# Kernel optimization log

Hardware: AMD Instinct MI355X
Metric: run time of the kernel (lower is better)

Reference implementation:

```python
import jax, jax.numpy as jnp
import numpy as np


def _quant_dequant_rowwise(v):
    # vector-wise absmax int8 quantization along the last axis, then dequant.
    # Exactly reproduces dequantized result of the int8 GEMM operand:
    # Cx = round(v/s) clipped to [-127,127]; dq = Cx * s.
    s = jnp.max(jnp.abs(v), axis=-1, keepdims=True) / 127.0
    s = jnp.maximum(s, 1e-8)
    q = jnp.clip(jnp.round(v / s), -127.0, 127.0)
    return q * s


def setup_inputs() -> dict:
    key = jax.random.key(0)
    k1, k2, k3 = jax.random.split(key, 3)
    B, S, K, N = 4, 2048, 4096, 4096
    x = jax.random.normal(k1, (B, S, K), dtype=jnp.float32)
    # amplify a few feature columns so |col| exceeds the 6.0 outlier threshold,
    # exercising the LLM.int8() mixed-precision decomposition path
    x = x.at[..., ::256].multiply(10.0)
    W = jax.random.normal(k2, (N, K), dtype=jnp.float32) * 0.02
    bias = jax.random.normal(k3, (N,), dtype=jnp.float32) * 0.01
    return {"x": x, "W": W, "bias": bias, "threshold": 6}


def reference(x, W, bias, threshold):
    # LLM.int8() matmul with outlier decomposition (bnb.matmul semantics):
    #  1. columns of x whose absmax > threshold are outliers -> fp16/fp32 path
    #  2. remaining x columns + full W are vector-wise int8 quantized, int8 GEMM,
    #     dequant with per-row scales (exactly equal to dq(x) @ dq(W).T)
    #  3. out = int8-part + x_outlier @ W_outlier.T + bias
    thr = jnp.asarray(threshold, dtype=x.dtype)
    B_shape = x.shape[:-1]
    K = x.shape[-1]
    x2 = x.reshape(-1, K)                                   # [M, K]
    colmax = jnp.max(jnp.abs(x2), axis=0)                   # [K]
    out_mask = (colmax > thr).astype(x.dtype)               # 1.0 on outlier cols
    x_int = x2 * (1.0 - out_mask)                           # zero outlier cols
    dq_x = _quant_dequant_rowwise(x_int)                    # [M, K]
    dq_w = _quant_dequant_rowwise(W)                        # [N, K]
    out = dq_x @ dq_w.T                                     # int8 GEMM, dequantized
    out = out + (x2 * out_mask) @ (W * out_mask).T          # fp outlier GEMM
    out = out + bias
    return out.reshape(*B_shape, W.shape[0])
```

## Files before the change

kernel.cpp:

```cpp
#include <hip/hip_runtime.h>

typedef unsigned short u16;
typedef unsigned char u8;
typedef unsigned int u32;
typedef __attribute__((ext_vector_type(4))) float f32x4;
typedef __attribute__((ext_vector_type(16))) float f32x16;
typedef __attribute__((ext_vector_type(8))) __bf16 bf16x8;
typedef __attribute__((ext_vector_type(4))) int i32x4;
typedef __attribute__((ext_vector_type(16))) int i32x16;

__device__ __forceinline__ u16 f2bf(float f) {
  u32 u = __float_as_uint(f);
  u32 r = (u + 0x7fffu + ((u >> 16) & 1u)) >> 16;
  return (u16)r;
}

__device__ __forceinline__ float load_thr(const int* p) {
  int iv = *p;
  float fv = __int_as_float(iv);
  if (fv >= 1.0f && fv <= 1.0e6f) return fv;
  return (float)iv;
}

__device__ __forceinline__ void gload_lds16(const void* g, void* l) {
  __builtin_amdgcn_global_load_lds(
      (const __attribute__((address_space(1))) void*)g,
      (__attribute__((address_space(3))) void*)l, 16, 0, 0);
}

__global__ void k_init_cm(u32* cm, int K) {
  int i = blockIdx.x * 256 + threadIdx.x;
  if (i < K) cm[i] = 0u;
}

__global__ __launch_bounds__(256) void k_colmax(const float* __restrict__ x,
                                                u32* __restrict__ cm, int M,
                                                int K, int rpb) {
  int c4 = blockIdx.x * 256 + threadIdx.x;
  int r0 = blockIdx.y * rpb;
  int r1 = r0 + rpb;
  if (r1 > M) r1 = M;
  f32x4 mx = {0.f, 0.f, 0.f, 0.f};
  for (int r = r0; r < r1; ++r) {
    f32x4 v = *(const f32x4*)&x[(size_t)r * K + (size_t)c4 * 4];
#pragma unroll
    for (int i = 0; i < 4; ++i) mx[i] = fmaxf(mx[i], fabsf(v[i]));
  }
#pragma unroll
  for (int i = 0; i < 4; ++i)
    atomicMax(&cm[c4 * 4 + i], __float_as_uint(mx[i]));
}

__global__ void k_ocols(const u32* __restrict__ cm, const int* __restrict__ thr_i,
                        int K, int* __restrict__ meta) {
  int lane = threadIdx.x;
  float thr = load_thr(thr_i);
  const float* cmf = (const float*)cm;
  int per = K >> 6;
  int base = lane * per;
  int c = 0;
  for (int i = 0; i < per; ++i) c += (cmf[base + i] > thr) ? 1 : 0;
  int inc = c;
  for (int off = 1; off < 64; off <<= 1) {
    int t = __shfl_up(inc, off);
    if (lane >= off) inc += t;
  }
  int excl = inc - c;
  int total = __shfl(inc, 63);
  if (lane == 0) meta[0] = total < 64 ? total : 64;
  int idx = excl;
  for (int i = 0; i < per; ++i) {
    if (cmf[base + i] > thr) {
      if (idx < 64) meta[1 + idx] = base + i;
      idx++;
    }
  }
  for (int j = total + lane; j < 64; j += 64) meta[1 + j] = -1;
}

__global__ __launch_bounds__(256) void k_quant8(
    const float* __restrict__ src, const u32* __restrict__ cm,
    const int* __restrict__ thr_i, const int* __restrict__ meta,
    char* __restrict__ qdst, float* __restrict__ sdst, u16* __restrict__ odst,
    int K, int zero_outlier) {
  int row = blockIdx.x;
  int tid = threadIdx.x;
  float thr = load_thr(thr_i);
  const float* sr = src + (size_t)row * K;
  const float* cmf = (const float*)cm;

  float v[16];
  u32 omask = 0;
  float lmax = 0.f;
#pragma unroll
  for (int j = 0; j < 4; ++j) {
    int c4 = j * 256 + tid;
    f32x4 val = *(const f32x4*)&sr[c4 * 4];
    f32x4 cv = *(const f32x4*)&cmf[c4 * 4];
#pragma unroll
    for (int i = 0; i < 4; ++i) {
      float xv = val[i];
      v[j * 4 + i] = xv;
      bool is_out = cv[i] > thr;
      if (is_out) omask |= 1u << (j * 4 + i);
      if (!is_out || !zero_outlier) lmax = fmaxf(lmax, fabsf(xv));
    }
  }
  float m = lmax;
#pragma unroll
  for (int off = 32; off >= 1; off >>= 1) m = fmaxf(m, __shfl_down(m, off));
  __shared__ float red[4];
  int lane = tid & 63, wv = tid >> 6;
  if (lane == 0) red[wv] = m;
  __syncthreads();
  float rm = fmaxf(fmaxf(red[0], red[1]), fmaxf(red[2], red[3]));
  float s = fmaxf(rm / 127.0f, 1e-8f);

  u32* qt = (u32*)qdst;
  size_t rowpart = (size_t)(row >> 5) * (K >> 5) * 256 + (size_t)(row & 31) * 8;
#pragma unroll
  for (int j = 0; j < 4; ++j) {
    int c4 = j * 256 + tid;
    u32 pk = 0;
#pragma unroll
    for (int i = 0; i < 4; ++i) {
      float xv = v[j * 4 + i];
      int iq;
      if (zero_outlier && (omask & (1u << (j * 4 + i)))) {
        iq = 0;
      } else {
        float q = rintf(xv / s);
        q = fminf(fmaxf(q, -127.f), 127.f);
        iq = (int)q;
      }
      pk |= ((u32)(u8)(char)iq) << (8 * i);
    }
    qt[rowpart + (size_t)(c4 >> 3) * 256 + (c4 & 7)] = pk;
  }
  if (tid == 0) sdst[row] = s;
  if (tid < 64) {
    int n_out = meta[0];
    int oc = meta[1 + tid];
    u16 ov = 0;
    if (tid < n_out && oc >= 0) ov = f2bf(sr[oc]);
    odst[(size_t)row * 64 + tid] = ov;
  }
}

__global__ __launch_bounds__(512, 2) void k_gemm_i8(
    const char* __restrict__ qx, const char* __restrict__ qw,
    const float* __restrict__ sx, const float* __restrict__ sw,
    const float* __restrict__ bias, const char* __restrict__ xo,
    const char* __restrict__ wo, float* __restrict__ out, int M, int N,
    int K) {
  extern __shared__ char lds_raw[];
  int tid = threadIdx.x;
  int lane = tid & 63, wave = tid >> 6;
  int wm = wave >> 1, wn = wave & 1;

  int nwg = gridDim.x, bid = blockIdx.x;
  int swzb = (bid & 7) * (nwg >> 3) + (bid >> 3);
  int nbn = N >> 8;
  int bm = swzb / nbn, bn = swzb % nbn;
  int r0 = bm << 8, c0 = bn << 8;
  int K32 = K >> 5;
  int lbyte = (lane & 31) * 32 + (lane >> 5) * 16;

  size_t bpart[4];
  int bg[4];
#pragma unroll
  for (int i = 0; i < 4; ++i) {
    int g = tid + i * 512;
    int b = g >> 6;
    int nb = b >> 2, kb = b & 3;
    bpart[i] = ((size_t)((c0 >> 5) + nb) * K32 + kb) * 1024 + (g & 63) * 16;
    bg[i] = g;
  }
#define STAGE_B(bufp, kt)                                                     \
  {                                                                           \
    _Pragma("unroll") for (int i = 0; i < 4; ++i)                             \
        gload_lds16(qw + bpart[i] + ((size_t)((kt) >> 5) << 10),              \
                    (bufp) + bg[i] * 16);                                     \
  }

  const char* abase0 = qx + ((size_t)((r0 >> 5) + wm * 2) * K32 << 10) + lbyte;
  const char* abase1 = abase0 + ((size_t)K32 << 10);
#define LOAD_A(ar, kt)                                                        \
  {                                                                           \
    _Pragma("unroll") for (int ks = 0; ks < 4; ++ks) {                        \
      ar[ks] = *(const i32x4*)(abase0 + ((size_t)(((kt) >> 5) + ks) << 10));  \
      ar[4 + ks] =                                                            \
          *(const i32x4*)(abase1 + ((size_t)(((kt) >> 5) + ks) << 10));       \
    }                                                                         \
  }

#define BFR(dst, bufp, nf, ks)                                                \
  dst = *(const i32x4*)((bufp) + ((((wn * 4 + (nf)) * 4 + (ks)) << 10)) +     \
                        lbyte);

#define MFI(q, nf, av, bv)                                                    \
  asm volatile("v_mfma_i32_32x32x32_i8 %0, %1, %2, %0"                        \
               : "+v"(acc[q][nf])                                             \
               : "v"(av), "v"(bv))

#define CLUST(ac, p)                                                          \
  {                                                                           \
    __builtin_amdgcn_s_setprio(1);                                            \
    _Pragma("unroll") for (int ks = 0; ks < 4; ++ks) {                        \
      MFI(0, 2 * (p), ac[ks], Bf[ks]);                                        \
      MFI(0, 2 * (p) + 1, ac[ks], Bf[4 + ks]);                                \
      MFI(1, 2 * (p), ac[4 + ks], Bf[ks]);                                    \
      MFI(1, 2 * (p) + 1, ac[4 + ks], Bf[4 + ks]);                            \
    }                                                                         \
    __builtin_amdgcn_s_setprio(0);                                            \
  }

#define TILE(bufc, bufn, ac, an, ktn)                                         \
  {                                                                           \
    STAGE_B(bufn, ktn);                                                       \
    LOAD_A(an, ktn);                                                          \
    __builtin_amdgcn_sched_barrier(0);                                        \
    i32x4 Bf[8];                                                              \
    BFR(Bf[0], bufc, 0, 0); BFR(Bf[1], bufc, 0, 1);                           \
    BFR(Bf[2], bufc, 0, 2); BFR(Bf[3], bufc, 0, 3);                           \
    BFR(Bf[4], bufc, 1, 0); BFR(Bf[5], bufc, 1, 1);                           \
    BFR(Bf[6], bufc, 1, 2); BFR(Bf[7], bufc, 1, 3);                           \
    CLUST(ac, 0);                                                             \
    BFR(Bf[0], bufc, 2, 0); BFR(Bf[1], bufc, 2, 1);                           \
    BFR(Bf[2], bufc, 2, 2); BFR(Bf[3], bufc, 2, 3);                           \
    BFR(Bf[4], bufc, 3, 0); BFR(Bf[5], bufc, 3, 1);                           \
    BFR(Bf[6], bufc, 3, 2); BFR(Bf[7], bufc, 3, 3);                           \
    CLUST(ac, 1);                                                             \
    asm volatile("s_waitcnt vmcnt(0)" ::: "memory");                          \
    __builtin_amdgcn_s_barrier();                                             \
  }

  char* buf0 = lds_raw;
  char* buf1 = lds_raw + 32768;
  i32x16 acc[2][4] = {};
  i32x4 aA[8], aB[8];

  STAGE_B(buf0, 0);
  LOAD_A(aA, 0);
  asm volatile("s_waitcnt vmcnt(0)" ::: "memory");
  __builtin_amdgcn_s_barrier();

  int nit = K / 256;
  for (int it = 0; it < nit; ++it) {
    int kt1 = it * 256 + 128;
    int kt2 = it * 256 + 256;
    kt2 = (kt2 < K) ? kt2 : 0;
    TILE(buf0, buf1, aA, aB, kt1);
    TILE(buf1, buf0, aB, aA, kt2);
  }

#pragma unroll
  for (int i = 0; i < 4; ++i) {
    int g = tid + i * 512;
    int rw = g >> 3;
    int cb = ((g & 7) ^ (rw & 7)) << 4;
    gload_lds16(xo + (size_t)(r0 + rw) * 128 + cb, lds_raw + g * 16);
    gload_lds16(wo + (size_t)(c0 + rw) * 128 + cb, lds_raw + 32768 + g * 16);
  }

  f32x16 facc[2][4];
  float swv[4], bv[4];
#pragma unroll
  for (int nf = 0; nf < 4; ++nf) {
    swv[nf] = sw[c0 + wn * 128 + nf * 32 + (lane & 31)];
    bv[nf] = bias[c0 + wn * 128 + nf * 32 + (lane & 31)];
  }
#pragma unroll
  for (int q = 0; q < 2; ++q) {
    int gmb = r0 + wm * 64 + q * 32 + 4 * (lane >> 5);
    f32x4 s4a = *(const f32x4*)&sx[gmb];
    f32x4 s4b = *(const f32x4*)&sx[gmb + 8];
    f32x4 s4c = *(const f32x4*)&sx[gmb + 16];
    f32x4 s4d = *(const f32x4*)&sx[gmb + 24];
#pragma unroll
    for (int reg = 0; reg < 16; ++reg) {
      float sxv = (reg < 4) ? s4a[reg & 3]
                : (reg < 8) ? s4b[reg & 3]
                : (reg < 12) ? s4c[reg & 3] : s4d[reg & 3];
#pragma unroll
      for (int nf = 0; nf < 4; ++nf)
        facc[q][nf][reg] = (float)acc[q][nf][reg] * sxv * swv[nf];
    }
  }

  asm volatile("s_waitcnt vmcnt(0)" ::: "memory");
  __builtin_amdgcn_s_barrier();

#pragma unroll
  for (int ks = 0; ks < 4; ++ks) {
    bf16x8 ob[4];
#pragma unroll
    for (int nf = 0; nf < 4; ++nf) {
      int rn = wn * 128 + nf * 32 + (lane & 31);
      ob[nf] = *(const bf16x8*)(lds_raw + 32768 + rn * 128 +
                                (((ks * 2 + (lane >> 5)) ^ (rn & 7)) << 4));
    }
#pragma unroll
    for (int q = 0; q < 2; ++q) {
      int rl = wm * 64 + q * 32 + (lane & 31);
      bf16x8 oa = *(const bf16x8*)(lds_raw + rl * 128 +
                                   (((ks * 2 + (lane >> 5)) ^ (rl & 7)) << 4));
#pragma unroll
      for (int nf = 0; nf < 4; ++nf)
        facc[q][nf] = __builtin_amdgcn_mfma_f32_32x32x16_bf16(
            oa, ob[nf], facc[q][nf], 0, 0, 0);
    }
  }

#pragma unroll
  for (int q = 0; q < 2; ++q) {
#pragma unroll
    for (int reg = 0; reg < 16; ++reg) {
      int gm = r0 + wm * 64 + q * 32 + (reg & 3) + 8 * (reg >> 2) +
               4 * (lane >> 5);
      float* orow = out + (size_t)gm * N + c0 + wn * 128 + (lane & 31);
#pragma unroll
      for (int nf = 0; nf < 4; ++nf)
        orow[nf * 32] = facc[q][nf][reg] + bv[nf];
    }
  }
}

extern "C" void kernel_launch(void* const* d_in, const int* in_sizes, int n_in,
                              void* d_out, int out_size, void* d_ws,
                              size_t ws_size, hipStream_t stream) {
  const float* x = (const float*)d_in[0];
  const float* W = (const float*)d_in[1];
  const float* bias = (const float*)d_in[2];
  const int* thr = (const int*)d_in[3];
  float* out = (float*)d_out;

  int N = in_sizes[2];
  int K = in_sizes[1] / N;
  int M = in_sizes[0] / K;

  char* ws = (char*)d_ws;
  u32* cm = (u32*)ws;
  int* meta = (int*)(ws + 16384);
  float* sx = (float*)(ws + 32768);
  float* sw = (float*)(ws + 32768 + (size_t)M * 4);
  char* xo = ws + 32768 + (size_t)(M + N) * 4;
  char* wo = xo + (size_t)M * 128;
  char* qx = wo + (size_t)N * 128;
  char* qw = qx + (size_t)M * K;

  k_init_cm<<<dim3((K + 255) / 256), dim3(256), 0, stream>>>(cm, K);

  {
    int gx = K / 1024;
    int gy = 128;
    int rpb = (M + gy - 1) / gy;
    k_colmax<<<dim3(gx, gy), dim3(256), 0, stream>>>(x, cm, M, K, rpb);
  }

  k_ocols<<<dim3(1), dim3(64), 0, stream>>>(cm, thr, K, meta);

  k_quant8<<<dim3(M), dim3(256), 0, stream>>>(x, cm, thr, meta, qx, sx,
                                              (u16*)xo, K, 1);
  k_quant8<<<dim3(N), dim3(256), 0, stream>>>(W, cm, thr, meta, qw, sw,
                                              (u16*)wo, K, 0);

  (void)hipFuncSetAttribute((const void*)k_gemm_i8,
                            hipFuncAttributeMaxDynamicSharedMemorySize,
                            65536);
  int nwg = (M / 256) * (N / 256);
  k_gemm_i8<<<dim3(nwg), dim3(512), 65536, stream>>>(qx, qw, sx, sw, bias,
                                                     xo, wo, out, M, N, K);
}
```

Baseline: 266.6 us.

## Shrink int8 GEMM tile to 128x256 with 2x4 waves and higher occupancy

Halves the M dimension of each int8 GEMM workgroup tile and rearranges the 8 waves as 2x4, so each wave owns a 64x64 output block with fewer accumulators. The launch bound now targets 4 workgroups per CU. A loads are no longer prefetched a whole tile ahead; they are issued inside each tile in two halves, with explicit waitcnt instructions to overlap them with the MFMAs. An XOR swizzle is added to the quantized operand layout, with matching read offsets, to cut LDS and register-load bank conflicts. The trade-off is twice as many workgroups and less register-level reuse per wave, in exchange for better latency hiding from higher occupancy.

```diff
diff --git a/kernel.cpp b/kernel.cpp
--- a/kernel.cpp
+++ b/kernel.cpp
@@ -118,6 +118,7 @@
 
   u32* qt = (u32*)qdst;
   size_t rowpart = (size_t)(row >> 5) * (K >> 5) * 256 + (size_t)(row & 31) * 8;
+  u32 wxor = ((row >> 2) & 1) << 2;
 #pragma unroll
   for (int j = 0; j < 4; ++j) {
     int c4 = j * 256 + tid;
@@ -135,7 +136,7 @@
       }
       pk |= ((u32)(u8)(char)iq) << (8 * i);
     }
-    qt[rowpart + (size_t)(c4 >> 3) * 256 + (c4 & 7)] = pk;
+    qt[rowpart + (size_t)(c4 >> 3) * 256 + ((c4 & 7) ^ wxor)] = pk;
   }
   if (tid == 0) sdst[row] = s;
   if (tid < 64) {
@@ -147,7 +148,7 @@
   }
 }
 
-__global__ __launch_bounds__(512, 2) void k_gemm_i8(
+__global__ __launch_bounds__(512, 4) void k_gemm_i8(
     const char* __restrict__ qx, const char* __restrict__ qw,
     const float* __restrict__ sx, const float* __restrict__ sw,
     const float* __restrict__ bias, const char* __restrict__ xo,
@@ -156,119 +157,125 @@
   extern __shared__ char lds_raw[];
   int tid = threadIdx.x;
   int lane = tid & 63, wave = tid >> 6;
-  int wm = wave >> 1, wn = wave & 1;
+  int wm = wave >> 2, wn = wave & 3;
 
   int nwg = gridDim.x, bid = blockIdx.x;
   int swzb = (bid & 7) * (nwg >> 3) + (bid >> 3);
   int nbn = N >> 8;
   int bm = swzb / nbn, bn = swzb % nbn;
-  int r0 = bm << 8, c0 = bn << 8;
+  int r0 = bm << 7, c0 = bn << 8;
   int K32 = K >> 5;
-  int lbyte = (lane & 31) * 32 + (lane >> 5) * 16;
-
-  size_t bpart[4];
+  int lbyte = (lane & 31) * 32 + ((((lane >> 5) ^ (lane >> 2)) & 1) << 4);
+
+  const char* bptr[4];
   int bg[4];
 #pragma unroll
   for (int i = 0; i < 4; ++i) {
     int g = tid + i * 512;
     int b = g >> 6;
     int nb = b >> 2, kb = b & 3;
-    bpart[i] = ((size_t)((c0 >> 5) + nb) * K32 + kb) * 1024 + (g & 63) * 16;
+    bptr[i] = qw + ((size_t)((c0 >> 5) + nb) * K32 + kb) * 1024 + (g & 63) * 16;
     bg[i] = g;
   }
 #define STAGE_B(bufp, kt)                                                     \
   {                                                                           \
     _Pragma("unroll") for (int i = 0; i < 4; ++i)                             \
-        gload_lds16(qw + bpart[i] + ((size_t)((kt) >> 5) << 10),              \
-                    (bufp) + bg[i] * 16);                                     \
+        gload_lds16(bptr[i] + ((size_t)((kt) >> 5) << 10), (bufp) + bg[i] * 16); \
   }
 
   const char* abase0 = qx + ((size_t)((r0 >> 5) + wm * 2) * K32 << 10) + lbyte;
   const char* abase1 = abase0 + ((size_t)K32 << 10);
-#define LOAD_A(ar, kt)                                                        \
-  {                                                                           \
-    _Pragma("unroll") for (int ks = 0; ks < 4; ++ks) {                        \
-      ar[ks] = *(const i32x4*)(abase0 + ((size_t)(((kt) >> 5) + ks) << 10));  \
-      ar[4 + ks] =                                                            \
-          *(const i32x4*)(abase1 + ((size_t)(((kt) >> 5) + ks) << 10));       \
-    }                                                                         \
-  }
-
-#define BFR(dst, bufp, nf, ks)                                                \
-  dst = *(const i32x4*)((bufp) + ((((wn * 4 + (nf)) * 4 + (ks)) << 10)) +     \
-                        lbyte);
+#define LDA2(aq, kt, ksA, ksB)                                                \
+  {                                                                           \
+    aq[0] = *(const i32x4*)(abase0 + ((size_t)(((kt) >> 5) + (ksA)) << 10));  \
+    aq[1] = *(const i32x4*)(abase1 + ((size_t)(((kt) >> 5) + (ksA)) << 10));  \
+    aq[2] = *(const i32x4*)(abase0 + ((size_t)(((kt) >> 5) + (ksB)) << 10));  \
+    aq[3] = *(const i32x4*)(abase1 + ((size_t)(((kt) >> 5) + (ksB)) << 10));  \
+  }
+
+#define BFR2(bq, bufp, ksA, ksB)                                              \
+  {                                                                           \
+    bq[0] = *(const i32x4*)((bufp) + (((wn * 2 + 0) * 4 + (ksA)) << 10) + lbyte); \
+    bq[1] = *(const i32x4*)((bufp) + (((wn * 2 + 1) * 4 + (ksA)) << 10) + lbyte); \
+    bq[2] = *(const i32x4*)((bufp) + (((wn * 2 + 0) * 4 + (ksB)) << 10) + lbyte); \
+    bq[3] = *(const i32x4*)((bufp) + (((wn * 2 + 1) * 4 + (ksB)) << 10) + lbyte); \
+  }
 
 #define MFI(q, nf, av, bv)                                                    \
   asm volatile("v_mfma_i32_32x32x32_i8 %0, %1, %2, %0"                        \
                : "+v"(acc[q][nf])                                             \
                : "v"(av), "v"(bv))
 
-#define CLUST(ac, p)                                                          \
+#define MH(aq, bq)                                                            \
   {                                                                           \
     __builtin_amdgcn_s_setprio(1);                                            \
-    _Pragma("unroll") for (int ks = 0; ks < 4; ++ks) {                        \
-      MFI(0, 2 * (p), ac[ks], Bf[ks]);                                        \
-      MFI(0, 2 * (p) + 1, ac[ks], Bf[4 + ks]);                                \
-      MFI(1, 2 * (p), ac[4 + ks], Bf[ks]);                                    \
-      MFI(1, 2 * (p) + 1, ac[4 + ks], Bf[4 + ks]);                            \
-    }                                                                         \
+    MFI(0, 0, aq[0], bq[0]);                                                  \
+    MFI(0, 1, aq[0], bq[1]);                                                  \
+    MFI(1, 0, aq[1], bq[0]);                                                  \
+    MFI(1, 1, aq[1], bq[1]);                                                  \
+    MFI(0, 0, aq[2], bq[2]);                                                  \
+    MFI(0, 1, aq[2], bq[3]);                                                  \
+    MFI(1, 0, aq[3], bq[2]);                                                  \
+    MFI(1, 1, aq[3], bq[3]);                                                  \
     __builtin_amdgcn_s_setprio(0);                                            \
   }
 
-#define TILE(bufc, bufn, ac, an, ktn)                                         \
-  {                                                                           \
+#define TILE(bufc, bufn, kt, ktn)                                             \
+  {                                                                           \
+    i32x4 aq[4], bq[4];                                                       \
+    LDA2(aq, kt, 0, 1);                                                       \
     STAGE_B(bufn, ktn);                                                       \
-    LOAD_A(an, ktn);                                                          \
-    __builtin_amdgcn_sched_barrier(0);                                        \
-    i32x4 Bf[8];                                                              \
-    BFR(Bf[0], bufc, 0, 0); BFR(Bf[1], bufc, 0, 1);                           \
-    BFR(Bf[2], bufc, 0, 2); BFR(Bf[3], bufc, 0, 3);                           \
-    BFR(Bf[4], bufc, 1, 0); BFR(Bf[5], bufc, 1, 1);                           \
-    BFR(Bf[6], bufc, 1, 2); BFR(Bf[7], bufc, 1, 3);                           \
-    CLUST(ac, 0);                                                             \
-    BFR(Bf[0], bufc, 2, 0); BFR(Bf[1], bufc, 2, 1);                           \
-    BFR(Bf[2], bufc, 2, 2); BFR(Bf[3], bufc, 2, 3);                           \
-    BFR(Bf[4], bufc, 3, 0); BFR(Bf[5], bufc, 3, 1);                           \
-    BFR(Bf[6], bufc, 3, 2); BFR(Bf[7], bufc, 3, 3);                           \
-    CLUST(ac, 1);                                                             \
+    BFR2(bq, bufc, 0, 1);                                                     \
+    asm volatile("s_waitcnt vmcnt(4)" ::: "memory");                          \
+    asm volatile("s_waitcnt lgkmcnt(0)" ::: "memory");                        \
+    MH(aq, bq);                                                               \
+    LDA2(aq, kt, 2, 3);                                                       \
+    BFR2(bq, bufc, 2, 3);                                                     \
     asm volatile("s_waitcnt vmcnt(0)" ::: "memory");                          \
+    asm volatile("s_waitcnt lgkmcnt(0)" ::: "memory");                        \
+    MH(aq, bq);                                                               \
     __builtin_amdgcn_s_barrier();                                             \
   }
 
   char* buf0 = lds_raw;
   char* buf1 = lds_raw + 32768;
-  i32x16 acc[2][4] = {};
-  i32x4 aA[8], aB[8];
+  i32x16 acc[2][2] = {};
 
   STAGE_B(buf0, 0);
-  LOAD_A(aA, 0);
   asm volatile("s_waitcnt vmcnt(0)" ::: "memory");
   __builtin_amdgcn_s_barrier();
 
   int nit = K / 256;
   for (int it = 0; it < nit; ++it) {
+    int kt0 = it * 256;
     int kt1 = it * 256 + 128;
     int kt2 = it * 256 + 256;
     kt2 = (kt2 < K) ? kt2 : 0;
-    TILE(buf0, buf1, aA, aB, kt1);
-    TILE(buf1, buf0, aB, aA, kt2);
-  }
-
+    TILE(buf0, buf1, kt0, kt1);
+    TILE(buf1, buf0, kt1, kt2);
+  }
+
+#pragma unroll
+  for (int i = 0; i < 2; ++i) {
+    int g = tid + i * 512;
+    int rw = g >> 3;
+    int cb = ((g & 7) ^ (rw & 7)) << 4;
+    gload_lds16(xo + (size_t)(r0 + rw) * 128 + cb, lds_raw + g * 16);
+  }
 #pragma unroll
   for (int i = 0; i < 4; ++i) {
     int g = tid + i * 512;
     int rw = g >> 3;
     int cb = ((g & 7) ^ (rw & 7)) << 4;
-    gload_lds16(xo + (size_t)(r0 + rw) * 128 + cb, lds_raw + g * 16);
-    gload_lds16(wo + (size_t)(c0 + rw) * 128 + cb, lds_raw + 32768 + g * 16);
-  }
-
-  f32x16 facc[2][4];
-  float swv[4], bv[4];
-#pragma unroll
-  for (int nf = 0; nf < 4; ++nf) {
-    swv[nf] = sw[c0 + wn * 128 + nf * 32 + (lane & 31)];
-    bv[nf] = bias[c0 + wn * 128 + nf * 32 + (lane & 31)];
+    gload_lds16(wo + (size_t)(c0 + rw) * 128 + cb, lds_raw + 16384 + g * 16);
+  }
+
+  f32x16 facc[2][2];
+  float swv[2], bv[2];
+#pragma unroll
+  for (int nf = 0; nf < 2; ++nf) {
+    swv[nf] = sw[c0 + wn * 64 + nf * 32 + (lane & 31)];
+    bv[nf] = bias[c0 + wn * 64 + nf * 32 + (lane & 31)];
   }
 #pragma unroll
   for (int q = 0; q < 2; ++q) {
@@ -283,7 +290,7 @@
                 : (reg < 8) ? s4b[reg & 3]
                 : (reg < 12) ? s4c[reg & 3] : s4d[reg & 3];
 #pragma unroll
-      for (int nf = 0; nf < 4; ++nf)
+      for (int nf = 0; nf < 2; ++nf)
         facc[q][nf][reg] = (float)acc[q][nf][reg] * sxv * swv[nf];
     }
   }
@@ -293,11 +300,11 @@
 
 #pragma unroll
   for (int ks = 0; ks < 4; ++ks) {
-    bf16x8 ob[4];
-#pragma unroll
-    for (int nf = 0; nf < 4; ++nf) {
-      int rn = wn * 128 + nf * 32 + (lane & 31);
-      ob[nf] = *(const bf16x8*)(lds_raw + 32768 + rn * 128 +
+    bf16x8 ob[2];
+#pragma unroll
+    for (int nf = 0; nf < 2; ++nf) {
+      int rn = wn * 64 + nf * 32 + (lane & 31);
+      ob[nf] = *(const bf16x8*)(lds_raw + 16384 + rn * 128 +
                                 (((ks * 2 + (lane >> 5)) ^ (rn & 7)) << 4));
     }
 #pragma unroll
@@ -306,7 +313,7 @@
       bf16x8 oa = *(const bf16x8*)(lds_raw + rl * 128 +
                                    (((ks * 2 + (lane >> 5)) ^ (rl & 7)) << 4));
 #pragma unroll
-      for (int nf = 0; nf < 4; ++nf)
+      for (int nf = 0; nf < 2; ++nf)
         facc[q][nf] = __builtin_amdgcn_mfma_f32_32x32x16_bf16(
             oa, ob[nf], facc[q][nf], 0, 0, 0);
     }
@@ -318,9 +325,9 @@
     for (int reg = 0; reg < 16; ++reg) {
       int gm = r0 + wm * 64 + q * 32 + (reg & 3) + 8 * (reg >> 2) +
                4 * (lane >> 5);
-      float* orow = out + (size_t)gm * N + c0 + wn * 128 + (lane & 31);
-#pragma unroll
-      for (int nf = 0; nf < 4; ++nf)
+      float* orow = out + (size_t)gm * N + c0 + wn * 64 + (lane & 31);
+#pragma unroll
+      for (int nf = 0; nf < 2; ++nf)
         orow[nf * 32] = facc[q][nf][reg] + bv[nf];
     }
   }
@@ -368,7 +375,7 @@
   (void)hipFuncSetAttribute((const void*)k_gemm_i8,
                             hipFuncAttributeMaxDynamicSharedMemorySize,
                             65536);
-  int nwg = (M / 256) * (N / 256);
+  int nwg = (M / 128) * (N / 256);
   k_gemm_i8<<<dim3(nwg), dim3(512), 65536, stream>>>(qx, qw, sx, sw, bias,
                                                      xo, wo, out, M, N, K);
 }
```

After: 288.4 us. +8.2%, slower.
